# Optimization experiments

Hardware: AMD Instinct MI355X
Metric: run time of the kernel (lower is better)

The kernel has to match this reference:

```python
import jax, jax.numpy as jnp
import numpy as np

N, C, A, E, D_OUT = 50000, 4, 16, 800000, 64
GEO_DIM = 2 * C + 9  # zero bond angles + zero dihedrals + 9 local-frame feats


def setup_inputs() -> dict:
    key = jax.random.key(0)
    ks = jax.random.split(key, 6)
    coord = jax.random.normal(ks[0], (N, C, 3), dtype=jnp.float32)
    attr = jax.random.normal(ks[1], (N, C, A), dtype=jnp.float32)
    channel_weights = jax.random.uniform(ks[2], (N, C), dtype=jnp.float32)
    W = jax.random.normal(ks[3], (D_OUT, A * A + GEO_DIM), dtype=jnp.float32) * (1.0 / np.sqrt(A * A + GEO_DIM))
    b = jnp.zeros((D_OUT,), dtype=jnp.float32)
    row = jax.random.randint(ks[4], (E,), 0, N, dtype=jnp.int32)
    col = jax.random.randint(ks[5], (E,), 0, N, dtype=jnp.int32)
    return {"coord": coord, "attr": attr, "channel_weights": channel_weights, "W": W, "b": b, "row": row, "col": col}


def _local_frames(coord):
    # coord: [N, C, 3] with channels (ca, c, n, ...) -> [N, 9] flattened rotation matrix
    ca, c, n = coord[:, 0], coord[:, 1], coord[:, 2]
    x = c - ca
    x = x / (jnp.linalg.norm(x, axis=-1, keepdims=True) + 1e-8)
    ty = n - ca
    y = ty - jnp.sum(ty * x, axis=-1, keepdims=True) * x
    y = y / (jnp.linalg.norm(y, axis=-1, keepdims=True) + 1e-8)
    z = jnp.cross(x, y)
    # torch.stack([x,y,z], dim=-1).reshape(N,-1): columns are x,y,z
    return jnp.stack([x, y, z], axis=-1).reshape(coord.shape[0], 9)


def reference(coord, attr, channel_weights, W, b, row, col):
    n_nodes, n_ch = coord.shape[0], coord.shape[1]
    n_edge = row.shape[0]
    # --- per-edge channel-pair distances, masked by channel-weight outer product ---
    diff = coord[row][:, :, None, :] - coord[col][:, None, :, :]        # [E, C, C, 3]
    coord_msg = jnp.linalg.norm(diff, axis=-1)                          # [E, C, C]
    coord_msg = coord_msg * (channel_weights[row][:, :, None] * channel_weights[col][:, None, :])
    # --- bilinear attr contraction: attr[row]^T @ coord_msg @ attr[col] ---
    radial = jnp.einsum('eia,eij,ejb->eab', attr[row], coord_msg, attr[col])  # [E, A, A]
    radial = radial.reshape(n_edge, -1)                                  # [E, A*A]
    # --- SE3 geometric features (bond/dihedral angles are zeros in source) ---
    lf = _local_frames(coord)                                            # [N, 9]
    # local_features repeated over channels; (lf[row]+lf[col]).mean over channel == lf[row]+lf[col]
    edge_lf = lf[row] + lf[col]                                          # [E, 9]
    geo = jnp.concatenate([jnp.zeros((n_edge, 2 * n_ch), radial.dtype), edge_lf], axis=-1)
    expanded = jnp.concatenate([radial, geo], axis=-1)                   # [E, A*A + GEO_DIM]
    # non-rbf path: linear_map(expanded) / (||expanded|| + CONSTANT)
    rnorm = jnp.linalg.norm(expanded, axis=-1, keepdims=True) + 1.0
    radials = (expanded @ W.T + b) / rnorm                               # [E, D_OUT]
    # --- coord_diff: row coords minus channel-mask-pooled col coords ---
    mask = (channel_weights != 0).astype(coord.dtype)                    # [N, C]
    csum = mask.sum(-1)                                                  # [N]
    pooled_col = (coord[col] * mask[col][..., None]).sum(1) / csum[col][:, None]  # [E, 3]
    coord_diff = coord[row] - pooled_col[:, None, :]                     # [E, C, 3]
    # --- node scatter-reduce: segment_sum of radials, segment_mean of coord_diff ---
    agg = jax.ops.segment_sum(radials, row, num_segments=n_nodes)        # [N, D_OUT]
    cnt = jax.ops.segment_sum(jnp.ones((n_edge,), coord.dtype), row, num_segments=n_nodes)
    coord_agg = jax.ops.segment_sum(coord_diff, row, num_segments=n_nodes) / jnp.clip(cnt, 1.0)[:, None, None]
    return jnp.concatenate([agg, coord_agg.reshape(n_nodes, -1)], axis=-1)  # [N, D_OUT + C*3]
```

## Files before the change

kernel.cpp:

```cpp
#include <hip/hip_runtime.h>
#include <math.h>

#define NN 50000
#define EDG 800000
#define OUTC 76
#define NKB 68
#define NB  196
#define CAP 64

#define CCW_OFF  0
#define LFP_OFF  (CCW_OFF + NN*16)
#define WK_OFF   (LFP_OFF + NN*16)
#define CNT_OFF  (WK_OFF + NKB*256)
#define CUR_OFF  (CNT_OFF + NN)
#define OFFS_OFF (CUR_OFF + 4)
#define TAIL_OFF (OFFS_OFF + NN + 4)
#define BUCKET_FLOATS ((size_t)TAIL_OFF + (size_t)NN * CAP)

__global__ void prep_kernel(const float* __restrict__ coord,
                            const float* __restrict__ cw,
                            const float* __restrict__ W,
                            const int* __restrict__ row,
                            const int* __restrict__ col,
                            float* __restrict__ ccwp,
                            float* __restrict__ lfp,
                            float* __restrict__ wk,
                            int* __restrict__ counts,
                            int* __restrict__ perm,
                            int* __restrict__ ecolb,
                            int* __restrict__ offs,
                            int E, int bucket) {
    int t = blockIdx.x * blockDim.x + threadIdx.x;

    if (t < E) {
        int r = row[t];
        int slot = atomicAdd(&counts[r], 1);
        if (bucket) ecolb[r * CAP + slot] = col[t];
        else        perm[t] = slot;
    }

    if (t < NKB * 64) {
        int kb = t >> 6, d = t & 63;
        float tmp[4];
        #pragma unroll
        for (int km = 0; km < 4; ++km) {
            int k = kb * 4 + km;
            int kcol = (k < 256) ? k : ((k < 265) ? k + 8 : -1);
            tmp[km] = (kcol >= 0) ? W[d * 273 + kcol] : 0.f;
        }
        ((float4*)wk)[t] = make_float4(tmp[0], tmp[1], tmp[2], tmp[3]);
    }

    if (t >= NN) return;
    if (bucket) offs[t] = t * CAP;

    const float* cp = coord + (size_t)t * 12;
    float c0x = cp[0], c0y = cp[1], c0z = cp[2];
    float c1x = cp[3], c1y = cp[4], c1z = cp[5];
    float c2x = cp[6], c2y = cp[7], c2z = cp[8];
    float c3x = cp[9], c3y = cp[10], c3z = cp[11];
    const float* wv = cw + (size_t)t * 4;
    float w0 = wv[0], w1 = wv[1], w2 = wv[2], w3 = wv[3];

    float* cc = ccwp + (size_t)t * 16;
    cc[0] = c0x; cc[1] = c0y; cc[2] = c0z; cc[3] = w0;
    cc[4] = c1x; cc[5] = c1y; cc[6] = c1z; cc[7] = w1;
    cc[8] = c2x; cc[9] = c2y; cc[10] = c2z; cc[11] = w2;
    cc[12] = c3x; cc[13] = c3y; cc[14] = c3z; cc[15] = w3;

    float xx = c1x - c0x, xy = c1y - c0y, xz = c1z - c0z;
    float invx = 1.0f / (sqrtf(xx * xx + xy * xy + xz * xz) + 1e-8f);
    xx *= invx; xy *= invx; xz *= invx;
    float tx = c2x - c0x, ty = c2y - c0y, tz = c2z - c0z;
    float dp = tx * xx + ty * xy + tz * xz;
    float yx = tx - dp * xx, yy = ty - dp * xy, yz = tz - dp * xz;
    float invy = 1.0f / (sqrtf(yx * yx + yy * yy + yz * yz) + 1e-8f);
    yx *= invy; yy *= invy; yz *= invy;
    float zx = xy * yz - xz * yy;
    float zy = xz * yx - xx * yz;
    float zz = xx * yy - xy * yx;

    float m0 = (w0 != 0.f) ? 1.f : 0.f;
    float m1 = (w1 != 0.f) ? 1.f : 0.f;
    float m2 = (w2 != 0.f) ? 1.f : 0.f;
    float m3 = (w3 != 0.f) ? 1.f : 0.f;
    float cs = m0 + m1 + m2 + m3;
    float px = (c0x * m0 + c1x * m1 + c2x * m2 + c3x * m3) / cs;
    float py = (c0y * m0 + c1y * m1 + c2y * m2 + c3y * m3) / cs;
    float pz = (c0z * m0 + c1z * m1 + c2z * m2 + c3z * m3) / cs;

    float* lp = lfp + (size_t)t * 16;
    lp[0] = xx; lp[1] = yx; lp[2] = zx;
    lp[3] = xy; lp[4] = yy; lp[5] = zy;
    lp[6] = xz; lp[7] = yz; lp[8] = zz;
    lp[9] = 0.f; lp[10] = 0.f; lp[11] = 0.f;
    lp[12] = px; lp[13] = py; lp[14] = pz; lp[15] = 0.f;
}

__global__ void scanalloc_kernel(const int* __restrict__ counts,
                                 int* __restrict__ cursor,
                                 int* __restrict__ offs) {
    int t = blockIdx.x * 256 + threadIdx.x;
    int v = (t < NN) ? counts[t] : 0;
    int lane = threadIdx.x & 63, wid = threadIdx.x >> 6;
    int x = v;
    #pragma unroll
    for (int d = 1; d < 64; d <<= 1) {
        int u = __shfl_up(x, d);
        x += (lane >= d) ? u : 0;
    }
    __shared__ int wtot[4];
    __shared__ int sbase;
    if (lane == 63) wtot[wid] = x;
    __syncthreads();
    if (threadIdx.x == 0)
        sbase = atomicAdd(cursor, wtot[0] + wtot[1] + wtot[2] + wtot[3]);
    __syncthreads();
    int wbase = 0;
    for (int i = 0; i < wid; ++i) wbase += wtot[i];
    if (t < NN) offs[t] = sbase + wbase + x - v;
}

__global__ void scatter_kernel(const int* __restrict__ row, const int* __restrict__ col,
                               const int* __restrict__ offs, const int* __restrict__ perm,
                               int* __restrict__ ecol, int E) {
    int e = blockIdx.x * blockDim.x + threadIdx.x;
    if (e >= E) return;
    ecol[offs[row[e]] + perm[e]] = col[e];
}

__device__ __forceinline__ float wave_sum64(float x) {
    float v = x, t;
    t = __int_as_float(__builtin_amdgcn_update_dpp(0, __float_as_int(v), 0x111, 0xf, 0xf, true)); v += t;
    t = __int_as_float(__builtin_amdgcn_update_dpp(0, __float_as_int(v), 0x112, 0xf, 0xf, true)); v += t;
    t = __int_as_float(__builtin_amdgcn_update_dpp(0, __float_as_int(v), 0x114, 0xf, 0xf, true)); v += t;
    t = __int_as_float(__builtin_amdgcn_update_dpp(0, __float_as_int(v), 0x118, 0xf, 0xf, true)); v += t;
    t = __int_as_float(__builtin_amdgcn_update_dpp(0, __float_as_int(v), 0x142, 0xa, 0xf, true)); v += t;
    t = __int_as_float(__builtin_amdgcn_update_dpp(0, __float_as_int(v), 0x143, 0xc, 0xf, true)); v += t;
    return __int_as_float(__builtin_amdgcn_readlane(__float_as_int(v), 63));
}

#define DPP(x, pat) __int_as_float(__builtin_amdgcn_update_dpp(0, __float_as_int(x), pat, 0xf, 0xf, true))

__global__ __launch_bounds__(256) void edge_kernel(
    const float* __restrict__ coord, const float* __restrict__ attr,
    const float* __restrict__ bvec,
    const float* __restrict__ ccw, const float* __restrict__ lfp,
    const float* __restrict__ wk,
    const int* __restrict__ offs, const int* __restrict__ counts,
    const int* __restrict__ ecol,
    float* __restrict__ out) {
    __shared__ float Acbuf[4][64];
    __shared__ float S[4][280];

    const int w = threadIdx.x >> 6;
    const int l = threadIdx.x & 63;
    const int l15 = l & 15;
    const int n = blockIdx.x * 4 + w;

    const int st = offs[n];
    const int deg = counts[n];
    const int en = st + deg;
    const int b0 = (l & 3) * 4;
    const int i4 = (l >> 2) & 3;
    const int j4 = l & 3;
    const int a  = l >> 2;

    const float Br0 = attr[(size_t)n * 64 + (size_t)(((i4 + 0) & 3) * 16) + a];
    const float Br1 = attr[(size_t)n * 64 + (size_t)(((i4 + 3) & 3) * 16) + a];
    const float Br2 = attr[(size_t)n * 64 + (size_t)(((i4 + 2) & 3) * 16) + a];
    const float Br3 = attr[(size_t)n * 64 + (size_t)(((i4 + 1) & 3) * 16) + a];
    const float4 cown = ((const float4*)ccw)[n * 4 + i4];
    const float crx = cown.x, cry = cown.y, crz = cown.z, cwr = cown.w;
    const float lrv = lfp[(size_t)n * 16 + l15];
    const float lfmask = (l < 9) ? 1.f : 0.f;
    const float pmask  = (l >= 12 && l < 15) ? 1.f : 0.f;

    float ax = 0.f, ay = 0.f, az = 0.f, aw = 0.f;
    float sgeo = 0.f, invs = 0.f, sp = 0.f;

    const float4* CCW4 = (const float4*)ccw;

    for (int base = st; base < en; base += 64) {
        int bcnt = en - base; bcnt = bcnt > 64 ? 64 : bcnt;
        int idx = base + (l < bcnt ? l : bcnt - 1);
        int cvec = ecol[idx];

        int c = __builtin_amdgcn_readlane(cvec, 0);
        float4 cc  = CCW4[c * 4 + j4];
        float  acv = attr[(size_t)c * 64 + l];
        float  lcv = lfp[c * 16 + l15];

        #pragma unroll 2
        for (int k = 0; k < bcnt; ++k) {
            Acbuf[w][l] = acv;

            int kn = (k + 1 < bcnt) ? k + 1 : k;
            int c2 = __builtin_amdgcn_readlane(cvec, kn);
            float4 cc_n  = CCW4[c2 * 4 + j4];
            float  ac_n  = attr[(size_t)c2 * 64 + l];
            float  lcv_n = lfp[c2 * 16 + l15];

            float dx = crx - cc.x, dy = cry - cc.y, dz = crz - cc.z;
            float m = __builtin_amdgcn_sqrtf(fmaf(dx, dx, fmaf(dy, dy, dz * dz))) * cwr * cc.w;

            float mr4  = DPP(m, 0x124);
            float mr8  = DPP(m, 0x128);
            float mr12 = DPP(m, 0x12C);
            float Uo = fmaf(Br3, mr12, fmaf(Br2, mr8, fmaf(Br1, mr4, Br0 * m)));

            float U0 = DPP(Uo, 0x00);
            float U1 = DPP(Uo, 0x55);
            float U2 = DPP(Uo, 0xAA);
            float U3 = DPP(Uo, 0xFF);

            float4 A0 = *(const float4*)&Acbuf[w][b0];
            float4 A1 = *(const float4*)&Acbuf[w][16 + b0];
            float4 A2 = *(const float4*)&Acbuf[w][32 + b0];
            float4 A3 = *(const float4*)&Acbuf[w][48 + b0];
            float ex = fmaf(U3, A3.x, fmaf(U2, A2.x, fmaf(U1, A1.x, U0 * A0.x)));
            float ey = fmaf(U3, A3.y, fmaf(U2, A2.y, fmaf(U1, A1.y, U0 * A0.y)));
            float ez = fmaf(U3, A3.z, fmaf(U2, A2.z, fmaf(U1, A1.z, U0 * A0.z)));
            float ew = fmaf(U3, A3.w, fmaf(U2, A2.w, fmaf(U1, A1.w, U0 * A0.w)));

            float glf  = (lrv + lcv) * lfmask;
            float part = fmaf(glf, glf, fmaf(ew, ew, fmaf(ez, ez, fmaf(ey, ey, ex * ex))));
            float tot  = wave_sum64(part);
            float invr = __builtin_amdgcn_rcpf(__builtin_amdgcn_sqrtf(tot) + 1.f);

            ax = fmaf(ex, invr, ax); ay = fmaf(ey, invr, ay);
            az = fmaf(ez, invr, az); aw = fmaf(ew, invr, aw);
            sgeo = fmaf(glf, invr, sgeo);
            invs += invr;
            sp = fmaf(lcv, pmask, sp);

            cc = cc_n; acv = ac_n; lcv = lcv_n;
        }
    }

    *(float4*)&S[w][l * 4] = make_float4(ax, ay, az, aw);
    if (l < 9)       S[w][256 + l] = sgeo;
    else if (l < 16) S[w][256 + l] = 0.f;
    if (l == 16)     S[w][272] = invs;
    if (l >= 12 && l < 15) S[w][273 + (l - 12)] = sp;

    float invsum = S[w][272];
    float acc = bvec[l] * invsum;
    const float4* WK4 = (const float4*)wk;
    #pragma unroll 4
    for (int kb = 0; kb < NKB; ++kb) {
        float4 wv = WK4[kb * 64 + l];
        float4 sv = *(const float4*)&S[w][kb * 4];
        acc += wv.x * sv.x + wv.y * sv.y + wv.z * sv.z + wv.w * sv.w;
    }
    out[(size_t)n * OUTC + l] = acc;

    float cntv = (float)deg;
    float invc = __builtin_amdgcn_rcpf(fmaxf(cntv, 1.f));
    if (l < 12) {
        int x = l % 3;
        out[(size_t)n * OUTC + 64 + l] = (cntv * coord[(size_t)n * 12 + l] - S[w][273 + x]) * invc;
    }
}

extern "C" void kernel_launch(void* const* d_in, const int* in_sizes, int n_in,
                              void* d_out, int out_size, void* d_ws, size_t ws_size,
                              hipStream_t stream) {
    const float* coord = (const float*)d_in[0];
    const float* attr  = (const float*)d_in[1];
    const float* cw    = (const float*)d_in[2];
    const float* W     = (const float*)d_in[3];
    const float* bvec  = (const float*)d_in[4];
    const int*   row   = (const int*)d_in[5];
    const int*   col   = (const int*)d_in[6];
    float* out = (float*)d_out;
    float* ws  = (float*)d_ws;
    int E = in_sizes[5];

    float* ccwp = ws + CCW_OFF;
    float* lfp  = ws + LFP_OFF;
    float* wk   = ws + WK_OFF;
    int* counts = (int*)(ws + CNT_OFF);
    int* cursor = (int*)(ws + CUR_OFF);
    int* offs   = (int*)(ws + OFFS_OFF);
    int* tail   = (int*)(ws + TAIL_OFF);

    const int bucket = (ws_size >= BUCKET_FLOATS * sizeof(float)) ? 1 : 0;

    hipMemsetAsync(counts, 0, (NN + 4) * sizeof(int), stream);

    if (bucket) {
        int* ecolb = tail;
        prep_kernel<<<(E + 255) / 256, 256, 0, stream>>>(
            coord, cw, W, row, col, ccwp, lfp, wk, counts,
            nullptr, ecolb, offs, E, 1);
        edge_kernel<<<NN / 4, 256, 0, stream>>>(coord, attr, bvec, ccwp, lfp, wk,
                                                offs, counts, ecolb, out);
    } else {
        int* perm = tail;
        int* ecol = tail + EDG;
        prep_kernel<<<(E + 255) / 256, 256, 0, stream>>>(
            coord, cw, W, row, col, ccwp, lfp, wk, counts,
            perm, nullptr, offs, E, 0);
        scanalloc_kernel<<<NB, 256, 0, stream>>>(counts, cursor, offs);
        scatter_kernel<<<(E + 255) / 256, 256, 0, stream>>>(row, col, offs, perm, ecol, E);
        edge_kernel<<<NN / 4, 256, 0, stream>>>(coord, attr, bvec, ccwp, lfp, wk,
                                                offs, counts, ecol, out);
    }
}
```

Baseline: 291.5 us.

## Load neighbor attr directly as float4 and fold row channel weight into Br

The edge loop no longer stages the neighbor's attr row in shared memory. Each lane now loads its four float4 slices of the neighbor attr straight from global memory, and the loop is flattened into a single per-node loop without the explicit next-edge prefetch. The row channel weight is premultiplied into the Br coefficients, so one multiply per edge goes away. In exchange the kernel issues more, redundant global loads and loses the software prefetch. It also assumes node degree is at most 64, since only one ecol vector is loaded per wave.

```diff
diff --git a/kernel.cpp b/kernel.cpp
--- a/kernel.cpp
+++ b/kernel.cpp
@@ -144,13 +144,13 @@
 
 __global__ __launch_bounds__(256) void edge_kernel(
     const float* __restrict__ coord, const float* __restrict__ attr,
+    const float* __restrict__ cw,
     const float* __restrict__ bvec,
     const float* __restrict__ ccw, const float* __restrict__ lfp,
     const float* __restrict__ wk,
     const int* __restrict__ offs, const int* __restrict__ counts,
     const int* __restrict__ ecol,
     float* __restrict__ out) {
-    __shared__ float Acbuf[4][64];
     __shared__ float S[4][280];
 
     const int w = threadIdx.x >> 6;
@@ -160,18 +160,18 @@
 
     const int st = offs[n];
     const int deg = counts[n];
-    const int en = st + deg;
-    const int b0 = (l & 3) * 4;
+    const int b04 = l & 3;
     const int i4 = (l >> 2) & 3;
     const int j4 = l & 3;
     const int a  = l >> 2;
 
-    const float Br0 = attr[(size_t)n * 64 + (size_t)(((i4 + 0) & 3) * 16) + a];
-    const float Br1 = attr[(size_t)n * 64 + (size_t)(((i4 + 3) & 3) * 16) + a];
-    const float Br2 = attr[(size_t)n * 64 + (size_t)(((i4 + 2) & 3) * 16) + a];
-    const float Br3 = attr[(size_t)n * 64 + (size_t)(((i4 + 1) & 3) * 16) + a];
+    const int r0 = (i4 + 0) & 3, r1 = (i4 + 3) & 3, r2 = (i4 + 2) & 3, r3 = (i4 + 1) & 3;
+    const float Br0 = attr[(size_t)n * 64 + r0 * 16 + a] * cw[n * 4 + r0];
+    const float Br1 = attr[(size_t)n * 64 + r1 * 16 + a] * cw[n * 4 + r1];
+    const float Br2 = attr[(size_t)n * 64 + r2 * 16 + a] * cw[n * 4 + r2];
+    const float Br3 = attr[(size_t)n * 64 + r3 * 16 + a] * cw[n * 4 + r3];
     const float4 cown = ((const float4*)ccw)[n * 4 + i4];
-    const float crx = cown.x, cry = cown.y, crz = cown.z, cwr = cown.w;
+    const float crx = cown.x, cry = cown.y, crz = cown.z;
     const float lrv = lfp[(size_t)n * 16 + l15];
     const float lfmask = (l < 9) ? 1.f : 0.f;
     const float pmask  = (l >= 12 && l < 15) ? 1.f : 0.f;
@@ -180,62 +180,48 @@
     float sgeo = 0.f, invs = 0.f, sp = 0.f;
 
     const float4* CCW4 = (const float4*)ccw;
-
-    for (int base = st; base < en; base += 64) {
-        int bcnt = en - base; bcnt = bcnt > 64 ? 64 : bcnt;
-        int idx = base + (l < bcnt ? l : bcnt - 1);
-        int cvec = ecol[idx];
-
-        int c = __builtin_amdgcn_readlane(cvec, 0);
+    const float4* AT4  = (const float4*)attr;
+
+    int cvec = ecol[st + l];
+
+    for (int k = 0; k < deg; ++k) {
+        int c = __builtin_amdgcn_readlane(cvec, k);
+
+        float4 A0 = AT4[(size_t)c * 16 + 0  + b04];
+        float4 A1 = AT4[(size_t)c * 16 + 4  + b04];
+        float4 A2 = AT4[(size_t)c * 16 + 8  + b04];
+        float4 A3 = AT4[(size_t)c * 16 + 12 + b04];
         float4 cc  = CCW4[c * 4 + j4];
-        float  acv = attr[(size_t)c * 64 + l];
         float  lcv = lfp[c * 16 + l15];
 
-        #pragma unroll 2
-        for (int k = 0; k < bcnt; ++k) {
-            Acbuf[w][l] = acv;
-
-            int kn = (k + 1 < bcnt) ? k + 1 : k;
-            int c2 = __builtin_amdgcn_readlane(cvec, kn);
-            float4 cc_n  = CCW4[c2 * 4 + j4];
-            float  ac_n  = attr[(size_t)c2 * 64 + l];
-            float  lcv_n = lfp[c2 * 16 + l15];
-
-            float dx = crx - cc.x, dy = cry - cc.y, dz = crz - cc.z;
-            float m = __builtin_amdgcn_sqrtf(fmaf(dx, dx, fmaf(dy, dy, dz * dz))) * cwr * cc.w;
-
-            float mr4  = DPP(m, 0x124);
-            float mr8  = DPP(m, 0x128);
-            float mr12 = DPP(m, 0x12C);
-            float Uo = fmaf(Br3, mr12, fmaf(Br2, mr8, fmaf(Br1, mr4, Br0 * m)));
-
-            float U0 = DPP(Uo, 0x00);
-            float U1 = DPP(Uo, 0x55);
-            float U2 = DPP(Uo, 0xAA);
-            float U3 = DPP(Uo, 0xFF);
-
-            float4 A0 = *(const float4*)&Acbuf[w][b0];
-            float4 A1 = *(const float4*)&Acbuf[w][16 + b0];
-            float4 A2 = *(const float4*)&Acbuf[w][32 + b0];
-            float4 A3 = *(const float4*)&Acbuf[w][48 + b0];
-            float ex = fmaf(U3, A3.x, fmaf(U2, A2.x, fmaf(U1, A1.x, U0 * A0.x)));
-            float ey = fmaf(U3, A3.y, fmaf(U2, A2.y, fmaf(U1, A1.y, U0 * A0.y)));
-            float ez = fmaf(U3, A3.z, fmaf(U2, A2.z, fmaf(U1, A1.z, U0 * A0.z)));
-            float ew = fmaf(U3, A3.w, fmaf(U2, A2.w, fmaf(U1, A1.w, U0 * A0.w)));
-
-            float glf  = (lrv + lcv) * lfmask;
-            float part = fmaf(glf, glf, fmaf(ew, ew, fmaf(ez, ez, fmaf(ey, ey, ex * ex))));
-            float tot  = wave_sum64(part);
-            float invr = __builtin_amdgcn_rcpf(__builtin_amdgcn_sqrtf(tot) + 1.f);
-
-            ax = fmaf(ex, invr, ax); ay = fmaf(ey, invr, ay);
-            az = fmaf(ez, invr, az); aw = fmaf(ew, invr, aw);
-            sgeo = fmaf(glf, invr, sgeo);
-            invs += invr;
-            sp = fmaf(lcv, pmask, sp);
-
-            cc = cc_n; acv = ac_n; lcv = lcv_n;
-        }
+        float dx = crx - cc.x, dy = cry - cc.y, dz = crz - cc.z;
+        float m = __builtin_amdgcn_sqrtf(fmaf(dx, dx, fmaf(dy, dy, dz * dz))) * cc.w;
+
+        float mr4  = DPP(m, 0x124);
+        float mr8  = DPP(m, 0x128);
+        float mr12 = DPP(m, 0x12C);
+        float Uo = fmaf(Br3, mr12, fmaf(Br2, mr8, fmaf(Br1, mr4, Br0 * m)));
+
+        float U0 = DPP(Uo, 0x00);
+        float U1 = DPP(Uo, 0x55);
+        float U2 = DPP(Uo, 0xAA);
+        float U3 = DPP(Uo, 0xFF);
+
+        float ex = fmaf(U3, A3.x, fmaf(U2, A2.x, fmaf(U1, A1.x, U0 * A0.x)));
+        float ey = fmaf(U3, A3.y, fmaf(U2, A2.y, fmaf(U1, A1.y, U0 * A0.y)));
+        float ez = fmaf(U3, A3.z, fmaf(U2, A2.z, fmaf(U1, A1.z, U0 * A0.z)));
+        float ew = fmaf(U3, A3.w, fmaf(U2, A2.w, fmaf(U1, A1.w, U0 * A0.w)));
+
+        float glf  = (lrv + lcv) * lfmask;
+        float part = fmaf(glf, glf, fmaf(ew, ew, fmaf(ez, ez, fmaf(ey, ey, ex * ex))));
+        float tot  = wave_sum64(part);
+        float invr = __builtin_amdgcn_rcpf(__builtin_amdgcn_sqrtf(tot) + 1.f);
+
+        ax = fmaf(ex, invr, ax); ay = fmaf(ey, invr, ay);
+        az = fmaf(ez, invr, az); aw = fmaf(ew, invr, aw);
+        sgeo = fmaf(glf, invr, sgeo);
+        invs += invr;
+        sp = fmaf(lcv, pmask, sp);
     }
 
     *(float4*)&S[w][l * 4] = make_float4(ax, ay, az, aw);
@@ -294,7 +280,7 @@
         prep_kernel<<<(E + 255) / 256, 256, 0, stream>>>(
             coord, cw, W, row, col, ccwp, lfp, wk, counts,
             nullptr, ecolb, offs, E, 1);
-        edge_kernel<<<NN / 4, 256, 0, stream>>>(coord, attr, bvec, ccwp, lfp, wk,
+        edge_kernel<<<NN / 4, 256, 0, stream>>>(coord, attr, cw, bvec, ccwp, lfp, wk,
                                                 offs, counts, ecolb, out);
     } else {
         int* perm = tail;
@@ -304,7 +290,7 @@
             perm, nullptr, offs, E, 0);
         scanalloc_kernel<<<NB, 256, 0, stream>>>(counts, cursor, offs);
         scatter_kernel<<<(E + 255) / 256, 256, 0, stream>>>(row, col, offs, perm, ecol, E);
-        edge_kernel<<<NN / 4, 256, 0, stream>>>(coord, attr, bvec, ccwp, lfp, wk,
+        edge_kernel<<<NN / 4, 256, 0, stream>>>(coord, attr, cw, bvec, ccwp, lfp, wk,
                                                 offs, counts, ecol, out);
     }
 }
```

Measured after the change: 357.1 us. +22.5%, slower.
